# Kernel optimization log

Measured on AMD Instinct MI355X. Metric: run time of the kernel, lower is better.

## Reference

```python
import jax, jax.numpy as jnp
import numpy as np

D = 768
SCALE = 1.0 / np.sqrt(D)  # 1/sqrt(question_size)
NEG_INF = -1e30


def setup_inputs() -> dict:
    key = jax.random.key(0)
    k1, k2, k3, k4 = jax.random.split(key, 4)
    B, Lc, Lq = 8, 2048, 1024
    context_hiddens = jax.random.normal(k1, (B, Lc, D), dtype=jnp.float32)
    context_mask = jnp.ones((B, Lc), dtype=jnp.float32)  # unused by forward (parity with original)
    question_hiddens = jax.random.normal(k2, (B, Lq, D), dtype=jnp.float32)
    question_mask = jax.random.randint(k3, (B, Lq), 0, 2, dtype=jnp.int32)
    # ensure at least one valid question token per row to avoid all -inf softmax
    question_mask = question_mask.at[:, 0].set(1)
    W = jax.random.normal(k4, (D, D), dtype=jnp.float32) * (1.0 / np.sqrt(D))
    b = jnp.zeros((D,), dtype=jnp.float32)
    return {
        "context_hiddens": context_hiddens,
        "context_mask": context_mask,
        "question_hiddens": question_hiddens,
        "question_mask": question_mask,
        "W": W,
        "b": b,
    }


def reference(context_hiddens, context_mask, question_hiddens, question_mask, W, b):
    # Linear projection of question hiddens: [B, Lq, D]
    query = jnp.einsum("bqd,ed->bqe", question_hiddens, W) + b
    # Bilinear scores: c_i' W q_j -> [B, Lc, Lq], scaled
    scores = jnp.einsum("bcd,bqd->bcq", context_hiddens, query) * SCALE
    # Masked softmax over question axis (mask==1 means valid)
    mask = question_mask[:, None, :].astype(jnp.bool_)  # [B, 1, Lq]
    scores = jnp.where(mask, scores, NEG_INF)
    attention_dist = jax.nn.softmax(scores, axis=2)
    # Weighted sum of question hiddens: [B, Lc, D]
    attn_output = jnp.einsum("bcq,bqd->bcd", attention_dist, question_hiddens)
    return jnp.concatenate([context_hiddens, attn_output], axis=2)  # [B, Lc, 2D]
```

## Files before the change

kernel.cpp:

```cpp
#include <hip/hip_runtime.h>
#include <hip/hip_bf16.h>
#include <cstdint>
#include <cstddef>

#define D 768
#define BATCH 8
#define LC 2048
#define LQ 1024
#define SCALE 0.03608439182435161f

typedef __attribute__((ext_vector_type(8))) short short8;
typedef __attribute__((ext_vector_type(4))) float floatx4;

__device__ __forceinline__ short f2bf(float f) {
    union { float f; uint32_t u; } v; v.f = f;
    uint32_t r = v.u + 0x7fffu + ((v.u >> 16) & 1u);
    return (short)(r >> 16);
}

__device__ __forceinline__ void gl_lds16(const short* g, short* l) {
    __builtin_amdgcn_global_load_lds(
        reinterpret_cast<const __attribute__((address_space(1))) unsigned int*>(
            reinterpret_cast<uintptr_t>(g)),
        reinterpret_cast<__attribute__((address_space(3))) unsigned int*>(
            reinterpret_cast<uintptr_t>(l)),
        16, 0, 0);
}

__device__ __forceinline__ void stage_tile(const short* gbase, int ld, int m0, int k0,
                                           short* lds, int tid) {
    const int r = tid >> 2, kc = (tid & 3) * 8;
    gl_lds16(gbase + (size_t)(m0 + r) * ld + k0 + kc, lds + tid * 8);
    gl_lds16(gbase + (size_t)(m0 + r + 64) * ld + k0 + kc, lds + 2048 + tid * 8);
}

__device__ __forceinline__ void mfma_tile_loop(
    const short* Ab, const short* Bb, int lda, int ldb, int K, int m0, int n0,
    short* sA, short* sB, int tid, floatx4 acc[4][4]) {
    const int w = tid >> 6, lane = tid & 63, l15 = lane & 15, quad = lane >> 4;
    const int wm = (w >> 1) * 64, wn = (w & 1) * 64;
    for (int k0 = 0; k0 < K; k0 += 32) {
        stage_tile(Ab, lda, m0, k0, sA, tid);
        stage_tile(Bb, ldb, n0, k0, sB, tid);
        __syncthreads();
        short8 af[4], bf[4];
#pragma unroll
        for (int mt = 0; mt < 4; ++mt)
            af[mt] = *reinterpret_cast<const short8*>(&sA[(wm + mt * 16 + l15) * 32 + quad * 8]);
#pragma unroll
        for (int nt = 0; nt < 4; ++nt)
            bf[nt] = *reinterpret_cast<const short8*>(&sB[(wn + nt * 16 + l15) * 32 + quad * 8]);
#pragma unroll
        for (int mt = 0; mt < 4; ++mt)
#pragma unroll
            for (int nt = 0; nt < 4; ++nt)
                acc[mt][nt] = __builtin_amdgcn_mfma_f32_16x16x32_bf16(af[mt], bf[nt], acc[mt][nt], 0, 0, 0);
        __syncthreads();
    }
}

__device__ __forceinline__ void gemm256_loop(
    const short* __restrict__ A, const short* __restrict__ B,
    int lda, int ldb, int K, int m0, int n0,
    short* lds, int tid, floatx4 acc[8][4]) {
    const int lane = tid & 63, l15 = lane & 15, quad = lane >> 4;
    const int w = tid >> 6, wm = w >> 2, wn = w & 3;

    const int c0 = tid, c1 = tid + 512;
    const int r0 = c0 >> 2, s0 = (c0 & 3) ^ (r0 & 3);
    const int r1 = c1 >> 2, s1 = (c1 & 3) ^ (r1 & 3);
    const short* gA0 = A + (size_t)(m0 + r0) * lda + s0 * 8;
    const short* gA1 = A + (size_t)(m0 + r1) * lda + s1 * 8;
    const short* gB0 = B + (size_t)(n0 + r0) * ldb + s0 * 8;
    const short* gB1 = B + (size_t)(n0 + r1) * ldb + s1 * 8;
    short* dA0 = lds + c0 * 8;
    short* dA1 = lds + c1 * 8;
    short* dB0 = lds + 8192 + c0 * 8;
    short* dB1 = lds + 8192 + c1 * 8;

    int aoff[8], boff[4];
#pragma unroll
    for (int mt = 0; mt < 8; ++mt) {
        int r = wm * 128 + mt * 16 + l15;
        aoff[mt] = r * 32 + ((quad ^ (r & 3)) * 8);
    }
#pragma unroll
    for (int nt = 0; nt < 4; ++nt) {
        int r = wn * 64 + nt * 16 + l15;
        boff[nt] = 8192 + r * 32 + ((quad ^ (r & 3)) * 8);
    }

    const int NT = K >> 5;
#define STAGE_A(t, bb) { gl_lds16(gA0 + (t) * 32, dA0 + (bb)); gl_lds16(gA1 + (t) * 32, dA1 + (bb)); }
#define STAGE_B(t, bb) { gl_lds16(gB0 + (t) * 32, dB0 + (bb)); gl_lds16(gB1 + (t) * 32, dB1 + (bb)); }
    STAGE_A(0, 0) STAGE_B(0, 0)
    STAGE_A(1, 16384) STAGE_B(1, 16384)

    for (int kt = 0; kt < NT; ++kt) {
        const int cur = (kt % 3) * 16384;
        const int nxt = ((kt + 2) % 3) * 16384;
        if (kt + 1 < NT) { asm volatile("s_waitcnt vmcnt(4)" ::: "memory"); }
        else             { asm volatile("s_waitcnt vmcnt(0)" ::: "memory"); }
        __builtin_amdgcn_s_barrier();

        if (kt + 2 < NT) STAGE_A((kt + 2), nxt)
        short8 af0[4], bf[4];
#pragma unroll
        for (int mt = 0; mt < 4; ++mt)
            af0[mt] = *reinterpret_cast<const short8*>(lds + cur + aoff[mt]);
#pragma unroll
        for (int nt = 0; nt < 4; ++nt)
            bf[nt] = *reinterpret_cast<const short8*>(lds + cur + boff[nt]);
        asm volatile("s_waitcnt lgkmcnt(0)" ::: "memory");
        __builtin_amdgcn_s_setprio(1);
#pragma unroll
        for (int mt = 0; mt < 4; ++mt)
#pragma unroll
            for (int nt = 0; nt < 4; ++nt)
                acc[mt][nt] = __builtin_amdgcn_mfma_f32_16x16x32_bf16(af0[mt], bf[nt], acc[mt][nt], 0, 0, 0);
        __builtin_amdgcn_s_setprio(0);
        __builtin_amdgcn_s_barrier();

        if (kt + 2 < NT) STAGE_B((kt + 2), nxt)
        short8 af1[4];
#pragma unroll
        for (int mt = 0; mt < 4; ++mt)
            af1[mt] = *reinterpret_cast<const short8*>(lds + cur + aoff[4 + mt]);
        asm volatile("s_waitcnt lgkmcnt(0)" ::: "memory");
        __builtin_amdgcn_s_setprio(1);
#pragma unroll
        for (int mt = 0; mt < 4; ++mt)
#pragma unroll
            for (int nt = 0; nt < 4; ++nt)
                acc[4 + mt][nt] = __builtin_amdgcn_mfma_f32_16x16x32_bf16(af1[mt], bf[nt], acc[4 + mt][nt], 0, 0, 0);
        __builtin_amdgcn_s_setprio(0);
    }
#undef STAGE_A
#undef STAGE_B
}

__global__ void cast_w_kernel(const float* __restrict__ src, short* __restrict__ dst,
                              float* __restrict__ sums) {
    int i = blockIdx.x * 256 + threadIdx.x;
    if (i < 4096) {
        float4 z = {0.f, 0.f, 0.f, 0.f};
        reinterpret_cast<float4*>(sums)[i] = z;
    }
    float4 v = reinterpret_cast<const float4*>(src)[i];
    short4 o;
    o.x = f2bf(v.x); o.y = f2bf(v.y); o.z = f2bf(v.z); o.w = f2bf(v.w);
    reinterpret_cast<short4*>(dst)[i] = o;
}

__global__ void qh_pass_kernel(const float* __restrict__ qh, short* __restrict__ qh_b,
                               short* __restrict__ qhT) {
    __shared__ float tile[32][33];
    const int b = blockIdx.z;
    const int q0 = blockIdx.x * 32, d0 = blockIdx.y * 32;
    const int t = threadIdx.x;
    const int r = t >> 3, c = (t & 7) * 4;
    const float4 v = *reinterpret_cast<const float4*>(qh + ((size_t)b * LQ + q0 + r) * D + d0 + c);
    tile[r][c] = v.x; tile[r][c + 1] = v.y; tile[r][c + 2] = v.z; tile[r][c + 3] = v.w;
    short4 d;
    d.x = f2bf(v.x); d.y = f2bf(v.y); d.z = f2bf(v.z); d.w = f2bf(v.w);
    *reinterpret_cast<short4*>(qh_b + ((size_t)b * LQ + q0 + r) * D + d0 + c) = d;
    __syncthreads();
    short4 o;
    o.x = f2bf(tile[c][r]); o.y = f2bf(tile[c + 1][r]);
    o.z = f2bf(tile[c + 2][r]); o.w = f2bf(tile[c + 3][r]);
    *reinterpret_cast<short4*>(qhT + ((size_t)b * D + d0 + r) * LQ + q0 + c) = o;
}

__global__ __launch_bounds__(256, 2) void gemm1_kernel(
    const short* __restrict__ A, const short* __restrict__ W,
    const float* __restrict__ bias, short* __restrict__ Q) {
    __shared__ short sA[128 * 32];
    __shared__ short sB[128 * 32];
    const int m0 = blockIdx.x * 128, n0 = blockIdx.y * 128;
    const int tid = threadIdx.x;
    const int w = tid >> 6, lane = tid & 63, l15 = lane & 15, quad = lane >> 4;
    const int wm = (w >> 1) * 64, wn = (w & 1) * 64;
    floatx4 acc[4][4];
#pragma unroll
    for (int i = 0; i < 4; ++i)
#pragma unroll
        for (int j = 0; j < 4; ++j) { floatx4 z = {0.f, 0.f, 0.f, 0.f}; acc[i][j] = z; }
    mfma_tile_loop(A, W, D, D, D, m0, n0, sA, sB, tid, acc);
    float bv[4];
#pragma unroll
    for (int nt = 0; nt < 4; ++nt) bv[nt] = bias[n0 + wn + nt * 16 + l15];
#pragma unroll
    for (int mt = 0; mt < 4; ++mt)
#pragma unroll
        for (int r = 0; r < 4; ++r) {
            int row = m0 + wm + mt * 16 + quad * 4 + r;
#pragma unroll
            for (int nt = 0; nt < 4; ++nt)
                Q[(size_t)row * D + n0 + wn + nt * 16 + l15] = f2bf(acc[mt][nt][r] + bv[nt]);
        }
}

__global__ void ctx_pass_kernel(const float* __restrict__ ctx, float* __restrict__ out,
                                short* __restrict__ ctxb) {
    size_t i = (size_t)blockIdx.x * 256 + threadIdx.x;
    size_t row = i / 192;
    size_t c4 = i % 192;
    float4 v = reinterpret_cast<const float4*>(ctx)[i];
    reinterpret_cast<float4*>(out)[row * 384 + c4] = v;
    short4 o;
    o.x = f2bf(v.x); o.y = f2bf(v.y); o.z = f2bf(v.z); o.w = f2bf(v.w);
    reinterpret_cast<short4*>(ctxb)[i] = o;
}

__global__ __launch_bounds__(512, 2) void scores256_kernel(
    const short* __restrict__ ctxb, const short* __restrict__ query_b,
    const int* __restrict__ qmask, short* __restrict__ P, float* __restrict__ sums) {
    __shared__ __align__(16) short lds[3 * 16384];
    const int nb = ((blockIdx.x & 7) << 5) + (blockIdx.x >> 3);
    const int b = nb >> 5, rem = nb & 31, by = rem >> 3, bx = rem & 7;
    const int m0 = bx << 8, n0 = by << 8;
    const int tid = threadIdx.x;
    const int lane = tid & 63, l15 = lane & 15, quad = lane >> 4;
    const int w = tid >> 6, wm = w >> 2, wn = w & 3;

    floatx4 acc[8][4];
#pragma unroll
    for (int i = 0; i < 8; ++i)
#pragma unroll
        for (int j = 0; j < 4; ++j) { floatx4 z = {0.f, 0.f, 0.f, 0.f}; acc[i][j] = z; }

    gemm256_loop(ctxb + (size_t)b * LC * D, query_b + (size_t)b * LQ * D,
                 D, D, D, m0, n0, lds, tid, acc);

    const int* mk = qmask + b * LQ;
    bool valid[4];
#pragma unroll
    for (int nt = 0; nt < 4; ++nt) valid[nt] = (mk[n0 + wn * 64 + nt * 16 + l15] != 0);
    short* Pb = P + (size_t)b * LC * LQ;
    float* sumb = sums + (size_t)b * LC;
#pragma unroll
    for (int mt = 0; mt < 8; ++mt)
#pragma unroll
        for (int rr = 0; rr < 4; ++rr) {
            int row = m0 + wm * 128 + mt * 16 + quad * 4 + rr;
            float psum = 0.f;
#pragma unroll
            for (int nt = 0; nt < 4; ++nt) {
                float pv = valid[nt] ? __expf(acc[mt][nt][rr] * SCALE) : 0.f;
                psum += pv;
                Pb[(size_t)row * LQ + n0 + wn * 64 + nt * 16 + l15] = f2bf(pv);
            }
#pragma unroll
            for (int off = 1; off < 16; off <<= 1)
                psum += __shfl_xor(psum, off, 64);
            if (l15 == 0)
                atomicAdd(&sumb[row], psum);
        }
}

__global__ __launch_bounds__(512, 2) void gemm2_256_kernel(
    const short* __restrict__ P, const short* __restrict__ qhT,
    const float* __restrict__ sums, float* __restrict__ out) {
    __shared__ __align__(16) short lds[3 * 16384];
    const int nb = (blockIdx.x & 7) * 24 + (blockIdx.x >> 3);
    const int b = nb / 24, rem = nb % 24, by = rem >> 3, bx = rem & 7;
    const int m0 = bx << 8, n0 = by << 8;
    const int tid = threadIdx.x;
    const int lane = tid & 63, l15 = lane & 15, quad = lane >> 4;
    const int w = tid >> 6, wm = w >> 2, wn = w & 3;

    floatx4 acc[8][4];
#pragma unroll
    for (int i = 0; i < 8; ++i)
#pragma unroll
        for (int j = 0; j < 4; ++j) { floatx4 z = {0.f, 0.f, 0.f, 0.f}; acc[i][j] = z; }

    gemm256_loop(P + (size_t)b * LC * LQ, qhT + (size_t)b * D * LQ,
                 LQ, LQ, LQ, m0, n0, lds, tid, acc);

    const float* sumb = sums + (size_t)b * LC;
#pragma unroll
    for (int mt = 0; mt < 8; ++mt)
#pragma unroll
        for (int rr = 0; rr < 4; ++rr) {
            int lrow = m0 + wm * 128 + mt * 16 + quad * 4 + rr;
            const float inv = 1.0f / sumb[lrow];
            size_t rowoff = ((size_t)b * LC + lrow) * 1536 + 768;
#pragma unroll
            for (int nt = 0; nt < 4; ++nt)
                out[rowoff + n0 + wn * 64 + nt * 16 + l15] = acc[mt][nt][rr] * inv;
        }
}

extern "C" void kernel_launch(void* const* d_in, const int* in_sizes, int n_in,
                              void* d_out, int out_size, void* d_ws, size_t ws_size,
                              hipStream_t stream) {
    const float* ctx = (const float*)d_in[0];
    const float* qh = (const float*)d_in[2];
    const int* qmask = (const int*)d_in[3];
    const float* Wf = (const float*)d_in[4];
    const float* bias = (const float*)d_in[5];
    float* out = (float*)d_out;

    char* ws = (char*)d_ws;
    short* W_b     = (short*)(ws);
    short* query_b = (short*)(ws + 1179648);
    short* qhT     = (short*)(ws + 13762560);
    short* ctx_b   = (short*)(ws + 26345472);
    short* P       = (short*)(ws + 51511296);
    float* sums    = (float*)(ws + 85065728);
    short* qh_b    = (short*)(ws + 51511296);

    cast_w_kernel<<<576, 256, 0, stream>>>(Wf, W_b, sums);
    qh_pass_kernel<<<dim3(32, 24, 8), 256, 0, stream>>>(qh, qh_b, qhT);
    ctx_pass_kernel<<<12288, 256, 0, stream>>>(ctx, out, ctx_b);
    gemm1_kernel<<<dim3(64, 6), 256, 0, stream>>>(qh_b, W_b, bias, query_b);
    scores256_kernel<<<dim3(256), dim3(512), 0, stream>>>(ctx_b, query_b, qmask, P, sums);
    gemm2_256_kernel<<<dim3(192), dim3(512), 0, stream>>>(P, qhT, sums, out);
}
```

Before: 266.6 us.

## Fuse all six kernels into one cooperative persistent kernel with grid syncs

```diff
diff --git a/kernel.cpp b/kernel.cpp
--- a/kernel.cpp
+++ b/kernel.cpp
@@ -1,7 +1,9 @@
 #include <hip/hip_runtime.h>
-#include <hip/hip_bf16.h>
+#include <hip/hip_cooperative_groups.h>
 #include <cstdint>
 #include <cstddef>
+
+namespace cg = cooperative_groups;
 
 #define D 768
 #define BATCH 8
@@ -25,38 +27,6 @@
         reinterpret_cast<__attribute__((address_space(3))) unsigned int*>(
             reinterpret_cast<uintptr_t>(l)),
         16, 0, 0);
-}
-
-__device__ __forceinline__ void stage_tile(const short* gbase, int ld, int m0, int k0,
-                                           short* lds, int tid) {
-    const int r = tid >> 2, kc = (tid & 3) * 8;
-    gl_lds16(gbase + (size_t)(m0 + r) * ld + k0 + kc, lds + tid * 8);
-    gl_lds16(gbase + (size_t)(m0 + r + 64) * ld + k0 + kc, lds + 2048 + tid * 8);
-}
-
-__device__ __forceinline__ void mfma_tile_loop(
-    const short* Ab, const short* Bb, int lda, int ldb, int K, int m0, int n0,
-    short* sA, short* sB, int tid, floatx4 acc[4][4]) {
-    const int w = tid >> 6, lane = tid & 63, l15 = lane & 15, quad = lane >> 4;
-    const int wm = (w >> 1) * 64, wn = (w & 1) * 64;
-    for (int k0 = 0; k0 < K; k0 += 32) {
-        stage_tile(Ab, lda, m0, k0, sA, tid);
-        stage_tile(Bb, ldb, n0, k0, sB, tid);
-        __syncthreads();
-        short8 af[4], bf[4];
-#pragma unroll
-        for (int mt = 0; mt < 4; ++mt)
-            af[mt] = *reinterpret_cast<const short8*>(&sA[(wm + mt * 16 + l15) * 32 + quad * 8]);
-#pragma unroll
-        for (int nt = 0; nt < 4; ++nt)
-            bf[nt] = *reinterpret_cast<const short8*>(&sB[(wn + nt * 16 + l15) * 32 + quad * 8]);
-#pragma unroll
-        for (int mt = 0; mt < 4; ++mt)
-#pragma unroll
-            for (int nt = 0; nt < 4; ++nt)
-                acc[mt][nt] = __builtin_amdgcn_mfma_f32_16x16x32_bf16(af[mt], bf[nt], acc[mt][nt], 0, 0, 0);
-        __syncthreads();
-    }
 }
 
 __device__ __forceinline__ void gemm256_loop(
@@ -91,10 +61,10 @@
     }
 
     const int NT = K >> 5;
-#define STAGE_A(t, bb) { gl_lds16(gA0 + (t) * 32, dA0 + (bb)); gl_lds16(gA1 + (t) * 32, dA1 + (bb)); }
-#define STAGE_B(t, bb) { gl_lds16(gB0 + (t) * 32, dB0 + (bb)); gl_lds16(gB1 + (t) * 32, dB1 + (bb)); }
-    STAGE_A(0, 0) STAGE_B(0, 0)
-    STAGE_A(1, 16384) STAGE_B(1, 16384)
+#define STAGE_A2(t, bb) { gl_lds16(gA0 + (t) * 32, dA0 + (bb)); gl_lds16(gA1 + (t) * 32, dA1 + (bb)); }
+#define STAGE_B2(t, bb) { gl_lds16(gB0 + (t) * 32, dB0 + (bb)); gl_lds16(gB1 + (t) * 32, dB1 + (bb)); }
+    STAGE_A2(0, 0) STAGE_B2(0, 0)
+    STAGE_A2(1, 16384) STAGE_B2(1, 16384)
 
     for (int kt = 0; kt < NT; ++kt) {
         const int cur = (kt % 3) * 16384;
@@ -103,7 +73,7 @@
         else             { asm volatile("s_waitcnt vmcnt(0)" ::: "memory"); }
         __builtin_amdgcn_s_barrier();
 
-        if (kt + 2 < NT) STAGE_A((kt + 2), nxt)
+        if (kt + 2 < NT) STAGE_A2((kt + 2), nxt)
         short8 af0[4], bf[4];
 #pragma unroll
         for (int mt = 0; mt < 4; ++mt)
@@ -121,7 +91,7 @@
         __builtin_amdgcn_s_setprio(0);
         __builtin_amdgcn_s_barrier();
 
-        if (kt + 2 < NT) STAGE_B((kt + 2), nxt)
+        if (kt + 2 < NT) STAGE_B2((kt + 2), nxt)
         short8 af1[4];
 #pragma unroll
         for (int mt = 0; mt < 4; ++mt)
@@ -135,161 +105,246 @@
                 acc[4 + mt][nt] = __builtin_amdgcn_mfma_f32_16x16x32_bf16(af1[mt], bf[nt], acc[4 + mt][nt], 0, 0, 0);
         __builtin_amdgcn_s_setprio(0);
     }
-#undef STAGE_A
-#undef STAGE_B
-}
-
-__global__ void cast_w_kernel(const float* __restrict__ src, short* __restrict__ dst,
-                              float* __restrict__ sums) {
-    int i = blockIdx.x * 256 + threadIdx.x;
-    if (i < 4096) {
-        float4 z = {0.f, 0.f, 0.f, 0.f};
-        reinterpret_cast<float4*>(sums)[i] = z;
-    }
-    float4 v = reinterpret_cast<const float4*>(src)[i];
-    short4 o;
-    o.x = f2bf(v.x); o.y = f2bf(v.y); o.z = f2bf(v.z); o.w = f2bf(v.w);
-    reinterpret_cast<short4*>(dst)[i] = o;
-}
-
-__global__ void qh_pass_kernel(const float* __restrict__ qh, short* __restrict__ qh_b,
-                               short* __restrict__ qhT) {
-    __shared__ float tile[32][33];
-    const int b = blockIdx.z;
-    const int q0 = blockIdx.x * 32, d0 = blockIdx.y * 32;
-    const int t = threadIdx.x;
-    const int r = t >> 3, c = (t & 7) * 4;
-    const float4 v = *reinterpret_cast<const float4*>(qh + ((size_t)b * LQ + q0 + r) * D + d0 + c);
-    tile[r][c] = v.x; tile[r][c + 1] = v.y; tile[r][c + 2] = v.z; tile[r][c + 3] = v.w;
-    short4 d;
-    d.x = f2bf(v.x); d.y = f2bf(v.y); d.z = f2bf(v.z); d.w = f2bf(v.w);
-    *reinterpret_cast<short4*>(qh_b + ((size_t)b * LQ + q0 + r) * D + d0 + c) = d;
-    __syncthreads();
-    short4 o;
-    o.x = f2bf(tile[c][r]); o.y = f2bf(tile[c + 1][r]);
-    o.z = f2bf(tile[c + 2][r]); o.w = f2bf(tile[c + 3][r]);
-    *reinterpret_cast<short4*>(qhT + ((size_t)b * D + d0 + r) * LQ + q0 + c) = o;
-}
-
-__global__ __launch_bounds__(256, 2) void gemm1_kernel(
-    const short* __restrict__ A, const short* __restrict__ W,
-    const float* __restrict__ bias, short* __restrict__ Q) {
-    __shared__ short sA[128 * 32];
-    __shared__ short sB[128 * 32];
-    const int m0 = blockIdx.x * 128, n0 = blockIdx.y * 128;
-    const int tid = threadIdx.x;
-    const int w = tid >> 6, lane = tid & 63, l15 = lane & 15, quad = lane >> 4;
-    const int wm = (w >> 1) * 64, wn = (w & 1) * 64;
-    floatx4 acc[4][4];
-#pragma unroll
-    for (int i = 0; i < 4; ++i)
-#pragma unroll
-        for (int j = 0; j < 4; ++j) { floatx4 z = {0.f, 0.f, 0.f, 0.f}; acc[i][j] = z; }
-    mfma_tile_loop(A, W, D, D, D, m0, n0, sA, sB, tid, acc);
-    float bv[4];
-#pragma unroll
-    for (int nt = 0; nt < 4; ++nt) bv[nt] = bias[n0 + wn + nt * 16 + l15];
-#pragma unroll
-    for (int mt = 0; mt < 4; ++mt)
-#pragma unroll
-        for (int r = 0; r < 4; ++r) {
-            int row = m0 + wm + mt * 16 + quad * 4 + r;
-#pragma unroll
-            for (int nt = 0; nt < 4; ++nt)
-                Q[(size_t)row * D + n0 + wn + nt * 16 + l15] = f2bf(acc[mt][nt][r] + bv[nt]);
-        }
-}
-
-__global__ void ctx_pass_kernel(const float* __restrict__ ctx, float* __restrict__ out,
-                                short* __restrict__ ctxb) {
-    size_t i = (size_t)blockIdx.x * 256 + threadIdx.x;
-    size_t row = i / 192;
-    size_t c4 = i % 192;
-    float4 v = reinterpret_cast<const float4*>(ctx)[i];
-    reinterpret_cast<float4*>(out)[row * 384 + c4] = v;
-    short4 o;
-    o.x = f2bf(v.x); o.y = f2bf(v.y); o.z = f2bf(v.z); o.w = f2bf(v.w);
-    reinterpret_cast<short4*>(ctxb)[i] = o;
-}
-
-__global__ __launch_bounds__(512, 2) void scores256_kernel(
-    const short* __restrict__ ctxb, const short* __restrict__ query_b,
-    const int* __restrict__ qmask, short* __restrict__ P, float* __restrict__ sums) {
-    __shared__ __align__(16) short lds[3 * 16384];
-    const int nb = ((blockIdx.x & 7) << 5) + (blockIdx.x >> 3);
-    const int b = nb >> 5, rem = nb & 31, by = rem >> 3, bx = rem & 7;
-    const int m0 = bx << 8, n0 = by << 8;
-    const int tid = threadIdx.x;
+#undef STAGE_A2
+#undef STAGE_B2
+}
+
+__device__ __forceinline__ void gemm256x128_loop(
+    const short* __restrict__ A, const short* __restrict__ B,
+    int lda, int ldb, int K, int m0, int n0,
+    short* lds, int tid, floatx4 acc[8][2]) {
     const int lane = tid & 63, l15 = lane & 15, quad = lane >> 4;
     const int w = tid >> 6, wm = w >> 2, wn = w & 3;
 
-    floatx4 acc[8][4];
-#pragma unroll
-    for (int i = 0; i < 8; ++i)
-#pragma unroll
-        for (int j = 0; j < 4; ++j) { floatx4 z = {0.f, 0.f, 0.f, 0.f}; acc[i][j] = z; }
-
-    gemm256_loop(ctxb + (size_t)b * LC * D, query_b + (size_t)b * LQ * D,
-                 D, D, D, m0, n0, lds, tid, acc);
-
-    const int* mk = qmask + b * LQ;
-    bool valid[4];
-#pragma unroll
-    for (int nt = 0; nt < 4; ++nt) valid[nt] = (mk[n0 + wn * 64 + nt * 16 + l15] != 0);
-    short* Pb = P + (size_t)b * LC * LQ;
-    float* sumb = sums + (size_t)b * LC;
-#pragma unroll
-    for (int mt = 0; mt < 8; ++mt)
-#pragma unroll
-        for (int rr = 0; rr < 4; ++rr) {
-            int row = m0 + wm * 128 + mt * 16 + quad * 4 + rr;
-            float psum = 0.f;
-#pragma unroll
-            for (int nt = 0; nt < 4; ++nt) {
-                float pv = valid[nt] ? __expf(acc[mt][nt][rr] * SCALE) : 0.f;
-                psum += pv;
-                Pb[(size_t)row * LQ + n0 + wn * 64 + nt * 16 + l15] = f2bf(pv);
+    const int c0 = tid, c1 = tid + 512;
+    const int r0 = c0 >> 2, s0 = (c0 & 3) ^ (r0 & 3);
+    const int r1 = c1 >> 2, s1 = (c1 & 3) ^ (r1 & 3);
+    const int rB = tid >> 2, sB = (tid & 3) ^ (rB & 3);
+    const short* gA0 = A + (size_t)(m0 + r0) * lda + s0 * 8;
+    const short* gA1 = A + (size_t)(m0 + r1) * lda + s1 * 8;
+    const short* gB0 = B + (size_t)(n0 + rB) * ldb + sB * 8;
+    short* dA0 = lds + c0 * 8;
+    short* dA1 = lds + c1 * 8;
+    short* dB0 = lds + 8192 + tid * 8;
+
+    int aoff[8], boff[2];
+#pragma unroll
+    for (int mt = 0; mt < 8; ++mt) {
+        int r = wm * 128 + mt * 16 + l15;
+        aoff[mt] = r * 32 + ((quad ^ (r & 3)) * 8);
+    }
+#pragma unroll
+    for (int nt = 0; nt < 2; ++nt) {
+        int r = wn * 32 + nt * 16 + l15;
+        boff[nt] = 8192 + r * 32 + ((quad ^ (r & 3)) * 8);
+    }
+
+    const int NT = K >> 5;
+#define STAGE_A1(t, bb) { gl_lds16(gA0 + (t) * 32, dA0 + (bb)); gl_lds16(gA1 + (t) * 32, dA1 + (bb)); }
+#define STAGE_B1(t, bb) { gl_lds16(gB0 + (t) * 32, dB0 + (bb)); }
+    STAGE_A1(0, 0) STAGE_B1(0, 0)
+    STAGE_A1(1, 12288) STAGE_B1(1, 12288)
+
+    for (int kt = 0; kt < NT; ++kt) {
+        const int cur = (kt % 3) * 12288;
+        const int nxt = ((kt + 2) % 3) * 12288;
+        if (kt + 1 < NT) { asm volatile("s_waitcnt vmcnt(3)" ::: "memory"); }
+        else             { asm volatile("s_waitcnt vmcnt(0)" ::: "memory"); }
+        __builtin_amdgcn_s_barrier();
+
+        if (kt + 2 < NT) STAGE_A1((kt + 2), nxt)
+        short8 af0[4], bf[2];
+#pragma unroll
+        for (int mt = 0; mt < 4; ++mt)
+            af0[mt] = *reinterpret_cast<const short8*>(lds + cur + aoff[mt]);
+#pragma unroll
+        for (int nt = 0; nt < 2; ++nt)
+            bf[nt] = *reinterpret_cast<const short8*>(lds + cur + boff[nt]);
+        asm volatile("s_waitcnt lgkmcnt(0)" ::: "memory");
+        __builtin_amdgcn_s_setprio(1);
+#pragma unroll
+        for (int mt = 0; mt < 4; ++mt)
+#pragma unroll
+            for (int nt = 0; nt < 2; ++nt)
+                acc[mt][nt] = __builtin_amdgcn_mfma_f32_16x16x32_bf16(af0[mt], bf[nt], acc[mt][nt], 0, 0, 0);
+        __builtin_amdgcn_s_setprio(0);
+        __builtin_amdgcn_s_barrier();
+
+        if (kt + 2 < NT) STAGE_B1((kt + 2), nxt)
+        short8 af1[4];
+#pragma unroll
+        for (int mt = 0; mt < 4; ++mt)
+            af1[mt] = *reinterpret_cast<const short8*>(lds + cur + aoff[4 + mt]);
+        asm volatile("s_waitcnt lgkmcnt(0)" ::: "memory");
+        __builtin_amdgcn_s_setprio(1);
+#pragma unroll
+        for (int mt = 0; mt < 4; ++mt)
+#pragma unroll
+            for (int nt = 0; nt < 2; ++nt)
+                acc[4 + mt][nt] = __builtin_amdgcn_mfma_f32_16x16x32_bf16(af1[mt], bf[nt], acc[4 + mt][nt], 0, 0, 0);
+        __builtin_amdgcn_s_setprio(0);
+    }
+#undef STAGE_A1
+#undef STAGE_B1
+}
+
+__global__ __launch_bounds__(512, 2) void mega_kernel(
+    const float* __restrict__ ctx, const float* __restrict__ qh,
+    const int* __restrict__ qmask, const float* __restrict__ Wf,
+    const float* __restrict__ bias, float* __restrict__ out,
+    short* __restrict__ W_b, short* __restrict__ query_b, short* __restrict__ qhT,
+    short* __restrict__ ctx_b, short* __restrict__ P, float* __restrict__ sums,
+    short* __restrict__ qh_b) {
+    __shared__ __align__(16) short lds[3 * 16384];
+    cg::grid_group grid = cg::this_grid();
+    const int tid = threadIdx.x;
+    const int bid = blockIdx.x;
+    const int gid = bid * 512 + tid;
+    const int nth = 256 * 512;
+
+    {
+        for (int i = gid; i < 147456; i += nth) {
+            float4 v = reinterpret_cast<const float4*>(Wf)[i];
+            short4 o;
+            o.x = f2bf(v.x); o.y = f2bf(v.y); o.z = f2bf(v.z); o.w = f2bf(v.w);
+            reinterpret_cast<short4*>(W_b)[i] = o;
+        }
+        for (int i = gid; i < 4096; i += nth) {
+            float4 z = {0.f, 0.f, 0.f, 0.f};
+            reinterpret_cast<float4*>(sums)[i] = z;
+        }
+        for (int i = gid; i < 3145728; i += nth) {
+            int row = i / 192, c4 = i % 192;
+            float4 v = reinterpret_cast<const float4*>(ctx)[i];
+            reinterpret_cast<float4*>(out)[(size_t)row * 384 + c4] = v;
+            short4 o;
+            o.x = f2bf(v.x); o.y = f2bf(v.y); o.z = f2bf(v.z); o.w = f2bf(v.w);
+            reinterpret_cast<short4*>(ctx_b)[i] = o;
+        }
+        float* tf = reinterpret_cast<float*>(lds);
+        float* mytile = tf + (tid >> 8) * (32 * 33);
+        const int st = tid & 255;
+        const int r = st >> 3, c = (st & 7) * 4;
+        for (int t2 = bid; t2 < 3072; t2 += 256) {
+            const int T = t2 * 2 + (tid >> 8);
+            const int b = T / 768, rem = T % 768;
+            const int q0 = (rem / 24) * 32, d0 = (rem % 24) * 32;
+            const float4 v = *reinterpret_cast<const float4*>(
+                qh + ((size_t)b * LQ + q0 + r) * D + d0 + c);
+            mytile[r * 33 + c] = v.x; mytile[r * 33 + c + 1] = v.y;
+            mytile[r * 33 + c + 2] = v.z; mytile[r * 33 + c + 3] = v.w;
+            short4 d;
+            d.x = f2bf(v.x); d.y = f2bf(v.y); d.z = f2bf(v.z); d.w = f2bf(v.w);
+            *reinterpret_cast<short4*>(qh_b + ((size_t)b * LQ + q0 + r) * D + d0 + c) = d;
+            __syncthreads();
+            short4 o;
+            o.x = f2bf(mytile[(c + 0) * 33 + r]); o.y = f2bf(mytile[(c + 1) * 33 + r]);
+            o.z = f2bf(mytile[(c + 2) * 33 + r]); o.w = f2bf(mytile[(c + 3) * 33 + r]);
+            *reinterpret_cast<short4*>(qhT + ((size_t)b * D + d0 + r) * LQ + q0 + c) = o;
+            __syncthreads();
+        }
+    }
+    __threadfence();
+    grid.sync();
+    __threadfence();
+
+    if (bid < 192) {
+        const int nb = (bid & 7) * 24 + (bid >> 3);
+        const int m0 = (nb / 6) * 256, n0 = (nb % 6) * 128;
+        const int lane = tid & 63, l15 = lane & 15, quad = lane >> 4;
+        const int w = tid >> 6, wm = w >> 2, wn = w & 3;
+        floatx4 acc[8][2];
+#pragma unroll
+        for (int i = 0; i < 8; ++i)
+#pragma unroll
+            for (int j = 0; j < 2; ++j) { floatx4 z = {0.f, 0.f, 0.f, 0.f}; acc[i][j] = z; }
+        gemm256x128_loop(qh_b, W_b, D, D, D, m0, n0, lds, tid, acc);
+        float bv[2];
+#pragma unroll
+        for (int nt = 0; nt < 2; ++nt) bv[nt] = bias[n0 + wn * 32 + nt * 16 + l15];
+#pragma unroll
+        for (int mt = 0; mt < 8; ++mt)
+#pragma unroll
+            for (int rr = 0; rr < 4; ++rr) {
+                int row = m0 + wm * 128 + mt * 16 + quad * 4 + rr;
+#pragma unroll
+                for (int nt = 0; nt < 2; ++nt)
+                    query_b[(size_t)row * D + n0 + wn * 32 + nt * 16 + l15] =
+                        f2bf(acc[mt][nt][rr] + bv[nt]);
             }
-#pragma unroll
-            for (int off = 1; off < 16; off <<= 1)
-                psum += __shfl_xor(psum, off, 64);
-            if (l15 == 0)
-                atomicAdd(&sumb[row], psum);
-        }
-}
-
-__global__ __launch_bounds__(512, 2) void gemm2_256_kernel(
-    const short* __restrict__ P, const short* __restrict__ qhT,
-    const float* __restrict__ sums, float* __restrict__ out) {
-    __shared__ __align__(16) short lds[3 * 16384];
-    const int nb = (blockIdx.x & 7) * 24 + (blockIdx.x >> 3);
-    const int b = nb / 24, rem = nb % 24, by = rem >> 3, bx = rem & 7;
-    const int m0 = bx << 8, n0 = by << 8;
-    const int tid = threadIdx.x;
-    const int lane = tid & 63, l15 = lane & 15, quad = lane >> 4;
-    const int w = tid >> 6, wm = w >> 2, wn = w & 3;
-
-    floatx4 acc[8][4];
-#pragma unroll
-    for (int i = 0; i < 8; ++i)
-#pragma unroll
-        for (int j = 0; j < 4; ++j) { floatx4 z = {0.f, 0.f, 0.f, 0.f}; acc[i][j] = z; }
-
-    gemm256_loop(P + (size_t)b * LC * LQ, qhT + (size_t)b * D * LQ,
-                 LQ, LQ, LQ, m0, n0, lds, tid, acc);
-
-    const float* sumb = sums + (size_t)b * LC;
-#pragma unroll
-    for (int mt = 0; mt < 8; ++mt)
-#pragma unroll
-        for (int rr = 0; rr < 4; ++rr) {
-            int lrow = m0 + wm * 128 + mt * 16 + quad * 4 + rr;
-            const float inv = 1.0f / sumb[lrow];
-            size_t rowoff = ((size_t)b * LC + lrow) * 1536 + 768;
-#pragma unroll
-            for (int nt = 0; nt < 4; ++nt)
-                out[rowoff + n0 + wn * 64 + nt * 16 + l15] = acc[mt][nt][rr] * inv;
-        }
+    }
+    __threadfence();
+    grid.sync();
+    __threadfence();
+
+    {
+        const int nb = ((bid & 7) << 5) + (bid >> 3);
+        const int b = nb >> 5, rem = nb & 31, by = rem >> 3, bx = rem & 7;
+        const int m0 = bx << 8, n0 = by << 8;
+        const int lane = tid & 63, l15 = lane & 15, quad = lane >> 4;
+        const int w = tid >> 6, wm = w >> 2, wn = w & 3;
+        floatx4 acc[8][4];
+#pragma unroll
+        for (int i = 0; i < 8; ++i)
+#pragma unroll
+            for (int j = 0; j < 4; ++j) { floatx4 z = {0.f, 0.f, 0.f, 0.f}; acc[i][j] = z; }
+        gemm256_loop(ctx_b + (size_t)b * LC * D, query_b + (size_t)b * LQ * D,
+                     D, D, D, m0, n0, lds, tid, acc);
+        const int* mk = qmask + b * LQ;
+        bool valid[4];
+#pragma unroll
+        for (int nt = 0; nt < 4; ++nt) valid[nt] = (mk[n0 + wn * 64 + nt * 16 + l15] != 0);
+        short* Pb = P + (size_t)b * LC * LQ;
+        float* sumb = sums + (size_t)b * LC;
+#pragma unroll
+        for (int mt = 0; mt < 8; ++mt)
+#pragma unroll
+            for (int rr = 0; rr < 4; ++rr) {
+                int row = m0 + wm * 128 + mt * 16 + quad * 4 + rr;
+                float psum = 0.f;
+#pragma unroll
+                for (int nt = 0; nt < 4; ++nt) {
+                    float pv = valid[nt] ? __expf(acc[mt][nt][rr] * SCALE) : 0.f;
+                    psum += pv;
+                    Pb[(size_t)row * LQ + n0 + wn * 64 + nt * 16 + l15] = f2bf(pv);
+                }
+#pragma unroll
+                for (int off = 1; off < 16; off <<= 1)
+                    psum += __shfl_xor(psum, off, 64);
+                if (l15 == 0)
+                    atomicAdd(&sumb[row], psum);
+            }
+    }
+    __threadfence();
+    grid.sync();
+    __threadfence();
+
+    if (bid < 192) {
+        const int nb = (bid & 7) * 24 + (bid >> 3);
+        const int b = nb / 24, rem = nb % 24, by = rem >> 3, bx = rem & 7;
+        const int m0 = bx << 8, n0 = by << 8;
+        const int lane = tid & 63, l15 = lane & 15, quad = lane >> 4;
+        const int w = tid >> 6, wm = w >> 2, wn = w & 3;
+        floatx4 acc[8][4];
+#pragma unroll
+        for (int i = 0; i < 8; ++i)
+#pragma unroll
+            for (int j = 0; j < 4; ++j) { floatx4 z = {0.f, 0.f, 0.f, 0.f}; acc[i][j] = z; }
+        gemm256_loop(P + (size_t)b * LC * LQ, qhT + (size_t)b * D * LQ,
+                     LQ, LQ, LQ, m0, n0, lds, tid, acc);
+        const float* sumb = sums + (size_t)b * LC;
+#pragma unroll
+        for (int mt = 0; mt < 8; ++mt)
+#pragma unroll
+            for (int rr = 0; rr < 4; ++rr) {
+                int lrow = m0 + wm * 128 + mt * 16 + quad * 4 + rr;
+                const float inv = 1.0f / sumb[lrow];
+                size_t rowoff = ((size_t)b * LC + lrow) * 1536 + 768;
+#pragma unroll
+                for (int nt = 0; nt < 4; ++nt)
+                    out[rowoff + n0 + wn * 64 + nt * 16 + l15] = acc[mt][nt][rr] * inv;
+            }
+    }
 }
 
 extern "C" void kernel_launch(void* const* d_in, const int* in_sizes, int n_in,
@@ -311,10 +366,8 @@
     float* sums    = (float*)(ws + 85065728);
     short* qh_b    = (short*)(ws + 51511296);
 
-    cast_w_kernel<<<576, 256, 0, stream>>>(Wf, W_b, sums);
-    qh_pass_kernel<<<dim3(32, 24, 8), 256, 0, stream>>>(qh, qh_b, qhT);
-    ctx_pass_kernel<<<12288, 256, 0, stream>>>(ctx, out, ctx_b);
-    gemm1_kernel<<<dim3(64, 6), 256, 0, stream>>>(qh_b, W_b, bias, query_b);
-    scores256_kernel<<<dim3(256), dim3(512), 0, stream>>>(ctx_b, query_b, qmask, P, sums);
-    gemm2_256_kernel<<<dim3(192), dim3(512), 0, stream>>>(P, qhT, sums, out);
-}
+    void* args[] = {(void*)&ctx, (void*)&qh, (void*)&qmask, (void*)&Wf, (void*)&bias,
+                    (void*)&out, (void*)&W_b, (void*)&query_b, (void*)&qhT, (void*)&ctx_b,
+                    (void*)&P, (void*)&sums, (void*)&qh_b};
+    hipLaunchCooperativeKernel(mega_kernel, dim3(256), dim3(512), args, 0, stream);
+}
```

New measurement: 642.0 us. 141% more time.
